# Performance work log

Measured on AMD Instinct MI355X. Metric: run time of the kernel, lower is better.

## Reference

```python
import jax, jax.numpy as jnp
import numpy as np

T, B, F, H, O = 512, 64, 128, 512, 16


def setup_inputs() -> dict:
    key = jax.random.key(0)
    ks = jax.random.split(key, 8)
    s = 1.0 / np.sqrt(H)  # torch RNN/Linear default uniform init scale
    u = lambda k, shape: jax.random.uniform(k, shape, jnp.float32, -s, s)
    return {
        "x_rnn": jax.random.normal(ks[0], (T, B, F), jnp.float32),
        "w_ih": u(ks[1], (3 * H, F)),   # gate order: r, z, n (PyTorch GRU)
        "w_hh": u(ks[2], (3 * H, H)),
        "b_ih": u(ks[3], (3 * H,)),
        "b_hh": u(ks[4], (3 * H,)),
        "w_out": u(ks[5], (O, H)),
        "b_out": u(ks[6], (O,)),
    }


def reference(x_rnn, w_ih, w_hh, b_ih, b_hh, w_out, b_out):
    # Single-layer GRU, seq-first (T, B, F), h0 = zeros (torch default when hx=None).
    h_dim = w_hh.shape[1]
    # Precompute all input-side gate pre-activations in one big GEMM: (T, B, 3H)
    xg = jnp.einsum("tbf,gf->tbg", x_rnn, w_ih) + b_ih

    def step(h, xg_t):
        hg = h @ w_hh.T + b_hh               # (B, 3H)
        xr, xz, xn = jnp.split(xg_t, 3, axis=-1)
        hr, hz, hn = jnp.split(hg, 3, axis=-1)
        r = jax.nn.sigmoid(xr + hr)
        z = jax.nn.sigmoid(xz + hz)
        n = jnp.tanh(xn + r * hn)
        h_new = (1.0 - z) * n + z * h
        return h_new, h_new

    h0 = jnp.zeros((x_rnn.shape[1], h_dim), x_rnn.dtype)
    _, hs = jax.lax.scan(step, h0, xg)       # hs: (T, B, H)
    # Output projection y = hs @ W_out^T + b_out -> (T, B, O)
    return jnp.einsum("tbh,oh->tbo", hs, w_out) + b_out
```

## Files before the change

kernel.cpp:

```cpp
#include <hip/hip_runtime.h>
#include <stdint.h>
#include <stddef.h>


#define T_LEN 512
#define B_SZ  64
#define F_DIM 128
#define H_DIM 512
#define O_DIM 16
#define SENTINEL 0xAAAAAAAAu

typedef __attribute__((ext_vector_type(8))) short short8;
typedef __attribute__((ext_vector_type(4))) float floatx4;
typedef __attribute__((ext_vector_type(4))) unsigned int uintx4;

__device__ __forceinline__ unsigned short f2bf(float f) {
  unsigned u = __builtin_bit_cast(unsigned, f);
  u += 0x7fffu + ((u >> 16) & 1u);
  return (unsigned short)(u >> 16);
}

__device__ __forceinline__ float fastrcp(float d) {
  float r = __builtin_amdgcn_rcpf(d);
  return r * (2.0f - d * r);
}

__device__ __forceinline__ float sigmoidf_(float x) {
  return fastrcp(1.0f + __expf(-x));
}

__device__ __forceinline__ float tanhf_(float x) {
  float v = fminf(fmaxf(x, -10.f), 10.f);
  float e = __expf(2.f * v);
  return (e - 1.f) * fastrcp(e + 1.f);
}

__device__ __forceinline__ short8 cvt8(floatx4 f0, floatx4 f1) {
  short8 a;
  a[0] = (short)f2bf(f0[0]); a[1] = (short)f2bf(f0[1]);
  a[2] = (short)f2bf(f0[2]); a[3] = (short)f2bf(f0[3]);
  a[4] = (short)f2bf(f1[0]); a[5] = (short)f2bf(f1[1]);
  a[6] = (short)f2bf(f1[2]); a[7] = (short)f2bf(f1[3]);
  return a;
}

__device__ __forceinline__ void hload4_sc1(floatx4* hf, const unsigned short* hbase) {
  asm volatile(
      "global_load_dwordx4 %0, %4, off sc1\n\t"
      "global_load_dwordx4 %1, %4, off offset:64 sc1\n\t"
      "global_load_dwordx4 %2, %4, off offset:128 sc1\n\t"
      "global_load_dwordx4 %3, %4, off offset:192 sc1\n\t"
      "s_waitcnt vmcnt(0)"
      : "=&v"(hf[0]), "=&v"(hf[1]), "=&v"(hf[2]), "=&v"(hf[3])
      : "v"(hbase)
      : "memory");
}

__global__ __launch_bounds__(256, 1)
void gru_persistent(const float* __restrict__ x,
                    const float* __restrict__ w_ih,
                    const float* __restrict__ w_hh,
                    const float* __restrict__ b_ih,
                    const float* __restrict__ b_hh,
                    unsigned short* __restrict__ hs) {
  __shared__ __align__(16) float part[2][4][16][33][4];

  const int tid  = threadIdx.x;
  const int lane = tid & 63;
  const int wv   = tid >> 6;
  const int bg   = blockIdx.x >> 4;
  const int cg   = blockIdx.x & 15;
  const int bgbase  = bg * 16;
  const int colbase = cg * 32;
  const int n16  = lane & 15;
  const int quad = lane >> 4;

  short8 bwx[3][2];
  short8 bwh[3][2][4];
  #pragma unroll
  for (int g = 0; g < 3; ++g) {
    #pragma unroll
    for (int nt = 0; nt < 2; ++nt) {
      const int grow = g * H_DIM + colbase + nt * 16 + n16;
      const float* pih = w_ih + (size_t)grow * F_DIM + wv * 32 + quad * 8;
      {
        short8 v;
        #pragma unroll
        for (int j = 0; j < 8; ++j) v[j] = (short)f2bf(pih[j]);
        bwx[g][nt] = v;
      }
      const float* phh = w_hh + (size_t)grow * H_DIM + wv * 128 + quad * 8;
      #pragma unroll
      for (int i = 0; i < 4; ++i) {
        short8 v;
        #pragma unroll
        for (int j = 0; j < 8; ++j) v[j] = (short)f2bf(phh[i * 32 + j]);
        bwh[g][nt][i] = v;
      }
    }
  }

  const int ew_b  = tid >> 4;
  const int ew_j0 = (tid & 15) * 2;
  float b_rz[2], b_zz[2], b_in[2], b_hn[2];
  #pragma unroll
  for (int e = 0; e < 2; ++e) {
    const int c = colbase + ew_j0 + e;
    b_rz[e] = b_ih[c] + b_hh[c];
    b_zz[e] = b_ih[H_DIM + c] + b_hh[H_DIM + c];
    b_in[e] = b_ih[2 * H_DIM + c];
    b_hn[e] = b_hh[2 * H_DIM + c];
  }
  float hm[2] = {0.0f, 0.0f};

  floatx4 xf0, xf1;
  {
    const float* px = x + ((size_t)(bgbase + n16)) * F_DIM + wv * 32 + quad * 8;
    xf0 = *(const floatx4*)px;
    xf1 = *(const floatx4*)(px + 4);
  }

  int mguard = 1 << 18;

  for (int t = 0; t < T_LEN; ++t) {
    floatx4 aR0 = {0.f,0.f,0.f,0.f}, aR1 = {0.f,0.f,0.f,0.f};
    floatx4 aZ0 = {0.f,0.f,0.f,0.f}, aZ1 = {0.f,0.f,0.f,0.f};
    floatx4 aX0 = {0.f,0.f,0.f,0.f}, aX1 = {0.f,0.f,0.f,0.f};
    floatx4 aH0 = {0.f,0.f,0.f,0.f}, aH1 = {0.f,0.f,0.f,0.f};
    {
      short8 a = cvt8(xf0, xf1);
      aR0 = __builtin_amdgcn_mfma_f32_16x16x32_bf16(a, bwx[0][0], aR0, 0, 0, 0);
      aR1 = __builtin_amdgcn_mfma_f32_16x16x32_bf16(a, bwx[0][1], aR1, 0, 0, 0);
      aZ0 = __builtin_amdgcn_mfma_f32_16x16x32_bf16(a, bwx[1][0], aZ0, 0, 0, 0);
      aZ1 = __builtin_amdgcn_mfma_f32_16x16x32_bf16(a, bwx[1][1], aZ1, 0, 0, 0);
      aX0 = __builtin_amdgcn_mfma_f32_16x16x32_bf16(a, bwx[2][0], aX0, 0, 0, 0);
      aX1 = __builtin_amdgcn_mfma_f32_16x16x32_bf16(a, bwx[2][1], aX1, 0, 0, 0);
    }

    if (t > 0) {
      floatx4 hf[4];
      {
        const unsigned short* hbase =
            hs + ((size_t)((t - 1) * B_SZ + bgbase + n16)) * H_DIM + wv * 128 + quad * 8;
        while (true) {
          hload4_sc1(hf, hbase);
          bool ok = true;
          #pragma unroll
          for (int i = 0; i < 4; ++i) {
            uintx4 u = __builtin_bit_cast(uintx4, hf[i]);
            ok = ok && (u[0] != SENTINEL) && (u[1] != SENTINEL) &&
                       (u[2] != SENTINEL) && (u[3] != SENTINEL);
          }
          if (__ballot(!ok) == 0ull) break;
          if (--mguard <= 0) break;
        }
      }
      if (t + 1 < T_LEN) {
        const float* px = x + ((size_t)((t + 1) * B_SZ + bgbase + n16)) * F_DIM +
                          wv * 32 + quad * 8;
        xf0 = *(const floatx4*)px;
        xf1 = *(const floatx4*)(px + 4);
      }
      #pragma unroll
      for (int i = 0; i < 4; ++i) {
        short8 a = __builtin_bit_cast(short8, hf[i]);
        aR0 = __builtin_amdgcn_mfma_f32_16x16x32_bf16(a, bwh[0][0][i], aR0, 0, 0, 0);
        aR1 = __builtin_amdgcn_mfma_f32_16x16x32_bf16(a, bwh[0][1][i], aR1, 0, 0, 0);
        aZ0 = __builtin_amdgcn_mfma_f32_16x16x32_bf16(a, bwh[1][0][i], aZ0, 0, 0, 0);
        aZ1 = __builtin_amdgcn_mfma_f32_16x16x32_bf16(a, bwh[1][1][i], aZ1, 0, 0, 0);
        aH0 = __builtin_amdgcn_mfma_f32_16x16x32_bf16(a, bwh[2][0][i], aH0, 0, 0, 0);
        aH1 = __builtin_amdgcn_mfma_f32_16x16x32_bf16(a, bwh[2][1][i], aH1, 0, 0, 0);
      }
    } else {
      const float* px = x + ((size_t)(B_SZ + bgbase + n16)) * F_DIM + wv * 32 + quad * 8;
      xf0 = *(const floatx4*)px;
      xf1 = *(const floatx4*)(px + 4);
    }

    {
      const int tb = t & 1;
      #pragma unroll
      for (int i = 0; i < 4; ++i) {
        const int r = quad * 4 + i;
        floatx4 v0 = {aR0[i], aZ0[i], aX0[i], aH0[i]};
        floatx4 v1 = {aR1[i], aZ1[i], aX1[i], aH1[i]};
        *(floatx4*)&part[tb][wv][r][n16][0]      = v0;
        *(floatx4*)&part[tb][wv][r][16 + n16][0] = v1;
      }
    }
    __syncthreads();

    {
      const int tb = t & 1;
      float pr[2] = {0.f, 0.f}, pz[2] = {0.f, 0.f};
      float pn[2] = {0.f, 0.f}, ph[2] = {0.f, 0.f};
      #pragma unroll
      for (int w = 0; w < 4; ++w) {
        #pragma unroll
        for (int e = 0; e < 2; ++e) {
          floatx4 g = *(const floatx4*)&part[tb][w][ew_b][ew_j0 + e][0];
          pr[e] += g[0]; pz[e] += g[1]; pn[e] += g[2]; ph[e] += g[3];
        }
      }
      unsigned short hb[2];
      #pragma unroll
      for (int e = 0; e < 2; ++e) {
        const float r = sigmoidf_(pr[e] + b_rz[e]);
        const float z = sigmoidf_(pz[e] + b_zz[e]);
        const float n = tanhf_(pn[e] + b_in[e] + r * (ph[e] + b_hn[e]));
        const float hn2 = (1.0f - z) * n + z * hm[e];
        hm[e] = hn2;
        hb[e] = f2bf(hn2);
      }
      const unsigned int packed = ((unsigned int)hb[1] << 16) | (unsigned int)hb[0];
      unsigned int* dst = (unsigned int*)(hs +
          ((size_t)(t * B_SZ + bgbase + ew_b)) * H_DIM + colbase + ew_j0);
      __hip_atomic_store(dst, packed, __ATOMIC_RELAXED, __HIP_MEMORY_SCOPE_AGENT);
    }
  }
}

__global__ __launch_bounds__(256, 1)
void gru_proj(const unsigned short* __restrict__ hs,
              const float* __restrict__ w_out,
              const float* __restrict__ b_out,
              float* __restrict__ y) {
  const int tid  = threadIdx.x;
  const int lane = tid & 63;
  const int wv   = tid >> 6;
  const int n16  = lane & 15;
  const int quad = lane >> 4;
  const size_t rowbase = ((size_t)blockIdx.x * 4 + wv) * 16;

  short8 bw[16];
  const float* pw = w_out + (size_t)n16 * H_DIM + quad * 8;
  #pragma unroll
  for (int kc = 0; kc < 16; ++kc) {
    short8 v;
    #pragma unroll
    for (int j = 0; j < 8; ++j) v[j] = (short)f2bf(pw[kc * 32 + j]);
    bw[kc] = v;
  }
  const float bo = b_out[n16];

  const unsigned short* hbase = hs + (rowbase + n16) * H_DIM + quad * 8;
  floatx4 acc = {0.f, 0.f, 0.f, 0.f};
  #pragma unroll
  for (int kc = 0; kc < 16; ++kc) {
    short8 a = *(const short8*)(hbase + kc * 32);
    acc = __builtin_amdgcn_mfma_f32_16x16x32_bf16(a, bw[kc], acc, 0, 0, 0);
  }
  #pragma unroll
  for (int i = 0; i < 4; ++i) {
    const size_t r = rowbase + quad * 4 + i;
    y[r * O_DIM + n16] = acc[i] + bo;
  }
}

extern "C" void kernel_launch(void* const* d_in, const int* in_sizes, int n_in,
                              void* d_out, int out_size, void* d_ws, size_t ws_size,
                              hipStream_t stream) {
  (void)in_sizes; (void)n_in; (void)out_size; (void)ws_size;
  const float* x     = (const float*)d_in[0];
  const float* w_ih  = (const float*)d_in[1];
  const float* w_hh  = (const float*)d_in[2];
  const float* b_ih  = (const float*)d_in[3];
  const float* b_hh  = (const float*)d_in[4];
  const float* w_out = (const float*)d_in[5];
  const float* b_out = (const float*)d_in[6];
  float* y = (float*)d_out;

  unsigned short* hs = (unsigned short*)d_ws;

  gru_persistent<<<64, 256, 0, stream>>>(x, w_ih, w_hh, b_ih, b_hh, hs);
  gru_proj<<<(T_LEN * B_SZ) / 16 / 4, 256, 0, stream>>>(hs, w_out, b_out, y);
}
```

Measured before the change: 1.080 ms.

## Interleave two batch groups per persistent block to hide cross-block sync latency

Halves the persistent grid so each block owns two 16-row batch groups. Each timestep now runs group A's step and then group B's step in alternation. While one group polls for the other blocks' hidden-state slices from the previous step, those producers have had a whole group-step of time to publish them. The aim is to hide the inter-block polling latency, at the cost of doubling the serial per-block work per timestep and using fewer CUs.

Result: slower. 1.831 ms (+69.6%).

```diff
diff --git a/kernel.cpp b/kernel.cpp
--- a/kernel.cpp
+++ b/kernel.cpp
@@ -13,6 +13,8 @@
 typedef __attribute__((ext_vector_type(8))) short short8;
 typedef __attribute__((ext_vector_type(4))) float floatx4;
 typedef __attribute__((ext_vector_type(4))) unsigned int uintx4;
+
+#define MFMA16(a, b, c) __builtin_amdgcn_mfma_f32_16x16x32_bf16((a), (b), (c), 0, 0, 0)
 
 __device__ __forceinline__ unsigned short f2bf(float f) {
   unsigned u = __builtin_bit_cast(unsigned, f);
@@ -56,24 +58,37 @@
       : "memory");
 }
 
+__device__ __forceinline__ bool clean4(const floatx4* hf) {
+  bool ok = true;
+  #pragma unroll
+  for (int i = 0; i < 4; ++i) {
+    uintx4 u = __builtin_bit_cast(uintx4, hf[i]);
+    ok = ok & (u[0] != SENTINEL) & (u[1] != SENTINEL) &
+         (u[2] != SENTINEL) & (u[3] != SENTINEL);
+  }
+  return __ballot(!ok) == 0ull;
+}
+
 __global__ __launch_bounds__(256, 1)
-void gru_persistent(const float* __restrict__ x,
-                    const float* __restrict__ w_ih,
-                    const float* __restrict__ w_hh,
-                    const float* __restrict__ b_ih,
-                    const float* __restrict__ b_hh,
-                    unsigned short* __restrict__ hs) {
+void gru_persistent2(const float* __restrict__ x,
+                     const float* __restrict__ w_ih,
+                     const float* __restrict__ w_hh,
+                     const float* __restrict__ b_ih,
+                     const float* __restrict__ b_hh,
+                     unsigned short* __restrict__ hs) {
   __shared__ __align__(16) float part[2][4][16][33][4];
 
   const int tid  = threadIdx.x;
   const int lane = tid & 63;
   const int wv   = tid >> 6;
-  const int bg   = blockIdx.x >> 4;
   const int cg   = blockIdx.x & 15;
-  const int bgbase  = bg * 16;
+  const int pair = blockIdx.x >> 4;
+  const int bgA  = pair * 32;
+  const int bgB  = bgA + 16;
   const int colbase = cg * 32;
   const int n16  = lane & 15;
   const int quad = lane >> 4;
+  const floatx4 fz = {0.f, 0.f, 0.f, 0.f};
 
   short8 bwx[3][2];
   short8 bwh[3][2][4];
@@ -111,111 +126,119 @@
     b_in[e] = b_ih[2 * H_DIM + c];
     b_hn[e] = b_hh[2 * H_DIM + c];
   }
-  float hm[2] = {0.0f, 0.0f};
-
-  floatx4 xf0, xf1;
+  float hmA[2] = {0.f, 0.f}, hmB[2] = {0.f, 0.f};
+
+  floatx4 xfA0, xfA1, xfB0, xfB1;
   {
-    const float* px = x + ((size_t)(bgbase + n16)) * F_DIM + wv * 32 + quad * 8;
-    xf0 = *(const floatx4*)px;
-    xf1 = *(const floatx4*)(px + 4);
-  }
-
+    const float* pa = x + ((size_t)(bgA + n16)) * F_DIM + wv * 32 + quad * 8;
+    xfA0 = *(const floatx4*)pa; xfA1 = *(const floatx4*)(pa + 4);
+    const float* pb = x + ((size_t)(bgB + n16)) * F_DIM + wv * 32 + quad * 8;
+    xfB0 = *(const floatx4*)pb; xfB1 = *(const floatx4*)(pb + 4);
+  }
+
+  floatx4 acc[8];
+  floatx4 hf[4];
   int mguard = 1 << 18;
 
-  for (int t = 0; t < T_LEN; ++t) {
-    floatx4 aR0 = {0.f,0.f,0.f,0.f}, aR1 = {0.f,0.f,0.f,0.f};
-    floatx4 aZ0 = {0.f,0.f,0.f,0.f}, aZ1 = {0.f,0.f,0.f,0.f};
-    floatx4 aX0 = {0.f,0.f,0.f,0.f}, aX1 = {0.f,0.f,0.f,0.f};
-    floatx4 aH0 = {0.f,0.f,0.f,0.f}, aH1 = {0.f,0.f,0.f,0.f};
-    {
-      short8 a = cvt8(xf0, xf1);
-      aR0 = __builtin_amdgcn_mfma_f32_16x16x32_bf16(a, bwx[0][0], aR0, 0, 0, 0);
-      aR1 = __builtin_amdgcn_mfma_f32_16x16x32_bf16(a, bwx[0][1], aR1, 0, 0, 0);
-      aZ0 = __builtin_amdgcn_mfma_f32_16x16x32_bf16(a, bwx[1][0], aZ0, 0, 0, 0);
-      aZ1 = __builtin_amdgcn_mfma_f32_16x16x32_bf16(a, bwx[1][1], aZ1, 0, 0, 0);
-      aX0 = __builtin_amdgcn_mfma_f32_16x16x32_bf16(a, bwx[2][0], aX0, 0, 0, 0);
-      aX1 = __builtin_amdgcn_mfma_f32_16x16x32_bf16(a, bwx[2][1], aX1, 0, 0, 0);
-    }
-
-    if (t > 0) {
-      floatx4 hf[4];
-      {
-        const unsigned short* hbase =
-            hs + ((size_t)((t - 1) * B_SZ + bgbase + n16)) * H_DIM + wv * 128 + quad * 8;
-        while (true) {
-          hload4_sc1(hf, hbase);
-          bool ok = true;
-          #pragma unroll
-          for (int i = 0; i < 4; ++i) {
-            uintx4 u = __builtin_bit_cast(uintx4, hf[i]);
-            ok = ok && (u[0] != SENTINEL) && (u[1] != SENTINEL) &&
-                       (u[2] != SENTINEL) && (u[3] != SENTINEL);
-          }
-          if (__ballot(!ok) == 0ull) break;
-          if (--mguard <= 0) break;
-        }
-      }
-      if (t + 1 < T_LEN) {
-        const float* px = x + ((size_t)((t + 1) * B_SZ + bgbase + n16)) * F_DIM +
-                          wv * 32 + quad * 8;
-        xf0 = *(const floatx4*)px;
-        xf1 = *(const floatx4*)(px + 4);
-      }
-      #pragma unroll
-      for (int i = 0; i < 4; ++i) {
-        short8 a = __builtin_bit_cast(short8, hf[i]);
-        aR0 = __builtin_amdgcn_mfma_f32_16x16x32_bf16(a, bwh[0][0][i], aR0, 0, 0, 0);
-        aR1 = __builtin_amdgcn_mfma_f32_16x16x32_bf16(a, bwh[0][1][i], aR1, 0, 0, 0);
-        aZ0 = __builtin_amdgcn_mfma_f32_16x16x32_bf16(a, bwh[1][0][i], aZ0, 0, 0, 0);
-        aZ1 = __builtin_amdgcn_mfma_f32_16x16x32_bf16(a, bwh[1][1][i], aZ1, 0, 0, 0);
-        aH0 = __builtin_amdgcn_mfma_f32_16x16x32_bf16(a, bwh[2][0][i], aH0, 0, 0, 0);
-        aH1 = __builtin_amdgcn_mfma_f32_16x16x32_bf16(a, bwh[2][1][i], aH1, 0, 0, 0);
-      }
-    } else {
-      const float* px = x + ((size_t)(B_SZ + bgbase + n16)) * F_DIM + wv * 32 + quad * 8;
-      xf0 = *(const floatx4*)px;
-      xf1 = *(const floatx4*)(px + 4);
-    }
-
-    {
-      const int tb = t & 1;
-      #pragma unroll
-      for (int i = 0; i < 4; ++i) {
-        const int r = quad * 4 + i;
-        floatx4 v0 = {aR0[i], aZ0[i], aX0[i], aH0[i]};
-        floatx4 v1 = {aR1[i], aZ1[i], aX1[i], aH1[i]};
-        *(floatx4*)&part[tb][wv][r][n16][0]      = v0;
-        *(floatx4*)&part[tb][wv][r][16 + n16][0] = v1;
-      }
+  auto xpart = [&](short8 a) {
+    acc[0] = MFMA16(a, bwx[0][0], fz); acc[1] = MFMA16(a, bwx[0][1], fz);
+    acc[2] = MFMA16(a, bwx[1][0], fz); acc[3] = MFMA16(a, bwx[1][1], fz);
+    acc[4] = MFMA16(a, bwx[2][0], fz); acc[5] = MFMA16(a, bwx[2][1], fz);
+    acc[6] = fz; acc[7] = fz;
+  };
+  auto hpart = [&]() {
+    #pragma unroll
+    for (int i = 0; i < 4; ++i) {
+      short8 a = __builtin_bit_cast(short8, hf[i]);
+      acc[0] = MFMA16(a, bwh[0][0][i], acc[0]); acc[1] = MFMA16(a, bwh[0][1][i], acc[1]);
+      acc[2] = MFMA16(a, bwh[1][0][i], acc[2]); acc[3] = MFMA16(a, bwh[1][1][i], acc[3]);
+      acc[6] = MFMA16(a, bwh[2][0][i], acc[6]); acc[7] = MFMA16(a, bwh[2][1][i], acc[7]);
+    }
+  };
+  auto epilogue = [&](int pb, int bgbase, float* hm2, int t) {
+    #pragma unroll
+    for (int i = 0; i < 4; ++i) {
+      const int r = quad * 4 + i;
+      floatx4 v0 = {acc[0][i], acc[2][i], acc[4][i], acc[6][i]};
+      floatx4 v1 = {acc[1][i], acc[3][i], acc[5][i], acc[7][i]};
+      *(floatx4*)&part[pb][wv][r][n16][0]      = v0;
+      *(floatx4*)&part[pb][wv][r][16 + n16][0] = v1;
     }
     __syncthreads();
-
-    {
-      const int tb = t & 1;
-      float pr[2] = {0.f, 0.f}, pz[2] = {0.f, 0.f};
-      float pn[2] = {0.f, 0.f}, ph[2] = {0.f, 0.f};
-      #pragma unroll
-      for (int w = 0; w < 4; ++w) {
-        #pragma unroll
-        for (int e = 0; e < 2; ++e) {
-          floatx4 g = *(const floatx4*)&part[tb][w][ew_b][ew_j0 + e][0];
-          pr[e] += g[0]; pz[e] += g[1]; pn[e] += g[2]; ph[e] += g[3];
-        }
-      }
-      unsigned short hb[2];
+    float pr[2] = {0.f, 0.f}, pz[2] = {0.f, 0.f};
+    float pn[2] = {0.f, 0.f}, ph[2] = {0.f, 0.f};
+    #pragma unroll
+    for (int w = 0; w < 4; ++w) {
       #pragma unroll
       for (int e = 0; e < 2; ++e) {
-        const float r = sigmoidf_(pr[e] + b_rz[e]);
-        const float z = sigmoidf_(pz[e] + b_zz[e]);
-        const float n = tanhf_(pn[e] + b_in[e] + r * (ph[e] + b_hn[e]));
-        const float hn2 = (1.0f - z) * n + z * hm[e];
-        hm[e] = hn2;
-        hb[e] = f2bf(hn2);
-      }
-      const unsigned int packed = ((unsigned int)hb[1] << 16) | (unsigned int)hb[0];
-      unsigned int* dst = (unsigned int*)(hs +
-          ((size_t)(t * B_SZ + bgbase + ew_b)) * H_DIM + colbase + ew_j0);
-      __hip_atomic_store(dst, packed, __ATOMIC_RELAXED, __HIP_MEMORY_SCOPE_AGENT);
+        floatx4 g = *(const floatx4*)&part[pb][w][ew_b][ew_j0 + e][0];
+        pr[e] += g[0]; pz[e] += g[1]; pn[e] += g[2]; ph[e] += g[3];
+      }
+    }
+    unsigned short hb2[2];
+    #pragma unroll
+    for (int e = 0; e < 2; ++e) {
+      const float r = sigmoidf_(pr[e] + b_rz[e]);
+      const float z = sigmoidf_(pz[e] + b_zz[e]);
+      const float n = tanhf_(pn[e] + b_in[e] + r * (ph[e] + b_hn[e]));
+      const float hn2 = (1.0f - z) * n + z * hm2[e];
+      hm2[e] = hn2;
+      hb2[e] = f2bf(hn2);
+    }
+    const unsigned int packed = ((unsigned int)hb2[1] << 16) | (unsigned int)hb2[0];
+    unsigned int* dst = (unsigned int*)(hs +
+        ((size_t)(t * B_SZ + bgbase + ew_b)) * H_DIM + colbase + ew_j0);
+    __hip_atomic_store(dst, packed, __ATOMIC_RELAXED, __HIP_MEMORY_SCOPE_AGENT);
+  };
+
+  xpart(cvt8(xfA0, xfA1));
+  {
+    const float* p = x + ((size_t)(B_SZ + bgA + n16)) * F_DIM + wv * 32 + quad * 8;
+    xfA0 = *(const floatx4*)p; xfA1 = *(const floatx4*)(p + 4);
+  }
+  epilogue(0, bgA, hmA, 0);
+
+  xpart(cvt8(xfB0, xfB1));
+  {
+    const float* p = x + ((size_t)(B_SZ + bgB + n16)) * F_DIM + wv * 32 + quad * 8;
+    xfB0 = *(const floatx4*)p; xfB1 = *(const floatx4*)(p + 4);
+  }
+  epilogue(1, bgB, hmB, 0);
+
+  for (int t = 1; t < T_LEN; ++t) {
+    {
+      xpart(cvt8(xfA0, xfA1));
+      const unsigned short* hb =
+          hs + ((size_t)((t - 1) * B_SZ + bgA + n16)) * H_DIM + wv * 128 + quad * 8;
+      while (true) {
+        hload4_sc1(hf, hb);
+        if (clean4(hf)) break;
+        if (--mguard <= 0) break;
+      }
+      if (t + 1 < T_LEN) {
+        const float* p = x + ((size_t)((t + 1) * B_SZ + bgA + n16)) * F_DIM +
+                         wv * 32 + quad * 8;
+        xfA0 = *(const floatx4*)p; xfA1 = *(const floatx4*)(p + 4);
+      }
+      hpart();
+      epilogue(0, bgA, hmA, t);
+    }
+    {
+      xpart(cvt8(xfB0, xfB1));
+      const unsigned short* hb =
+          hs + ((size_t)((t - 1) * B_SZ + bgB + n16)) * H_DIM + wv * 128 + quad * 8;
+      while (true) {
+        hload4_sc1(hf, hb);
+        if (clean4(hf)) break;
+        if (--mguard <= 0) break;
+      }
+      if (t + 1 < T_LEN) {
+        const float* p = x + ((size_t)((t + 1) * B_SZ + bgB + n16)) * F_DIM +
+                         wv * 32 + quad * 8;
+        xfB0 = *(const floatx4*)p; xfB1 = *(const floatx4*)(p + 4);
+      }
+      hpart();
+      epilogue(1, bgB, hmB, t);
     }
   }
 }
@@ -248,7 +271,7 @@
   #pragma unroll
   for (int kc = 0; kc < 16; ++kc) {
     short8 a = *(const short8*)(hbase + kc * 32);
-    acc = __builtin_amdgcn_mfma_f32_16x16x32_bf16(a, bw[kc], acc, 0, 0, 0);
+    acc = MFMA16(a, bw[kc], acc);
   }
   #pragma unroll
   for (int i = 0; i < 4; ++i) {
@@ -272,6 +295,6 @@
 
   unsigned short* hs = (unsigned short*)d_ws;
 
-  gru_persistent<<<64, 256, 0, stream>>>(x, w_ih, w_hh, b_ih, b_hh, hs);
+  gru_persistent2<<<32, 256, 0, stream>>>(x, w_ih, w_hh, b_ih, b_hh, hs);
   gru_proj<<<(T_LEN * B_SZ) / 16 / 4, 256, 0, stream>>>(hs, w_out, b_out, y);
 }
```

## Remap blocks to XCD slots and try cheaper sc0 polling before sc1

Applied to the files above, without the earlier changes.

Launches 128 blocks but keeps only those whose index mod 8 is below 4. Each batch group's column blocks then land on the same XCD under round-robin dispatch, which is meant to keep h exchange within one L2. The poll loop first tries up to three sc0 loads and clean checks before falling back to sc1 loads. It turns sc0 off after step 6 if it rarely succeeds. Each h store is also issued a second time with a plain global_store_dword, which adds memory traffic and relies on the hardware block-to-XCD mapping assumption.

Result: slower. 1.643 ms (+52.2%).

```diff
diff --git a/kernel.cpp b/kernel.cpp
--- a/kernel.cpp
+++ b/kernel.cpp
@@ -13,6 +13,8 @@
 typedef __attribute__((ext_vector_type(8))) short short8;
 typedef __attribute__((ext_vector_type(4))) float floatx4;
 typedef __attribute__((ext_vector_type(4))) unsigned int uintx4;
+
+#define MFMA16(a, b, c) __builtin_amdgcn_mfma_f32_16x16x32_bf16((a), (b), (c), 0, 0, 0)
 
 __device__ __forceinline__ unsigned short f2bf(float f) {
   unsigned u = __builtin_bit_cast(unsigned, f);
@@ -56,6 +58,29 @@
       : "memory");
 }
 
+__device__ __forceinline__ void hload4_sc0(floatx4* hf, const unsigned short* hbase) {
+  asm volatile(
+      "global_load_dwordx4 %0, %4, off sc0\n\t"
+      "global_load_dwordx4 %1, %4, off offset:64 sc0\n\t"
+      "global_load_dwordx4 %2, %4, off offset:128 sc0\n\t"
+      "global_load_dwordx4 %3, %4, off offset:192 sc0\n\t"
+      "s_waitcnt vmcnt(0)"
+      : "=&v"(hf[0]), "=&v"(hf[1]), "=&v"(hf[2]), "=&v"(hf[3])
+      : "v"(hbase)
+      : "memory");
+}
+
+__device__ __forceinline__ bool clean4(const floatx4* hf) {
+  bool ok = true;
+  #pragma unroll
+  for (int i = 0; i < 4; ++i) {
+    uintx4 u = __builtin_bit_cast(uintx4, hf[i]);
+    ok = ok & (u[0] != SENTINEL) & (u[1] != SENTINEL) &
+         (u[2] != SENTINEL) & (u[3] != SENTINEL);
+  }
+  return __ballot(!ok) == 0ull;
+}
+
 __global__ __launch_bounds__(256, 1)
 void gru_persistent(const float* __restrict__ x,
                     const float* __restrict__ w_ih,
@@ -63,13 +88,16 @@
                     const float* __restrict__ b_ih,
                     const float* __restrict__ b_hh,
                     unsigned short* __restrict__ hs) {
+  const int slot = (int)blockIdx.x & 7;
+  if (slot >= 4) return;
+
   __shared__ __align__(16) float part[2][4][16][33][4];
 
   const int tid  = threadIdx.x;
   const int lane = tid & 63;
   const int wv   = tid >> 6;
-  const int bg   = blockIdx.x >> 4;
-  const int cg   = blockIdx.x & 15;
+  const int bg   = slot;
+  const int cg   = (int)blockIdx.x >> 3;
   const int bgbase  = bg * 16;
   const int colbase = cg * 32;
   const int n16  = lane & 15;
@@ -120,7 +148,9 @@
     xf1 = *(const floatx4*)(px + 4);
   }
 
-  int mguard = 1 << 18;
+  int mguard  = 1 << 18;
+  int use_sc0 = 1;
+  int s0wins  = 0;
 
   for (int t = 0; t < T_LEN; ++t) {
     floatx4 aR0 = {0.f,0.f,0.f,0.f}, aR1 = {0.f,0.f,0.f,0.f};
@@ -129,12 +159,9 @@
     floatx4 aH0 = {0.f,0.f,0.f,0.f}, aH1 = {0.f,0.f,0.f,0.f};
     {
       short8 a = cvt8(xf0, xf1);
-      aR0 = __builtin_amdgcn_mfma_f32_16x16x32_bf16(a, bwx[0][0], aR0, 0, 0, 0);
-      aR1 = __builtin_amdgcn_mfma_f32_16x16x32_bf16(a, bwx[0][1], aR1, 0, 0, 0);
-      aZ0 = __builtin_amdgcn_mfma_f32_16x16x32_bf16(a, bwx[1][0], aZ0, 0, 0, 0);
-      aZ1 = __builtin_amdgcn_mfma_f32_16x16x32_bf16(a, bwx[1][1], aZ1, 0, 0, 0);
-      aX0 = __builtin_amdgcn_mfma_f32_16x16x32_bf16(a, bwx[2][0], aX0, 0, 0, 0);
-      aX1 = __builtin_amdgcn_mfma_f32_16x16x32_bf16(a, bwx[2][1], aX1, 0, 0, 0);
+      aR0 = MFMA16(a, bwx[0][0], aR0); aR1 = MFMA16(a, bwx[0][1], aR1);
+      aZ0 = MFMA16(a, bwx[1][0], aZ0); aZ1 = MFMA16(a, bwx[1][1], aZ1);
+      aX0 = MFMA16(a, bwx[2][0], aX0); aX1 = MFMA16(a, bwx[2][1], aX1);
     }
 
     if (t > 0) {
@@ -142,17 +169,22 @@
       {
         const unsigned short* hbase =
             hs + ((size_t)((t - 1) * B_SZ + bgbase + n16)) * H_DIM + wv * 128 + quad * 8;
+        bool won0 = false;
+        int tries = use_sc0 ? 3 : 0;
         while (true) {
-          hload4_sc1(hf, hbase);
-          bool ok = true;
-          #pragma unroll
-          for (int i = 0; i < 4; ++i) {
-            uintx4 u = __builtin_bit_cast(uintx4, hf[i]);
-            ok = ok && (u[0] != SENTINEL) && (u[1] != SENTINEL) &&
-                       (u[2] != SENTINEL) && (u[3] != SENTINEL);
+          if (tries > 0) {
+            --tries;
+            hload4_sc0(hf, hbase);
+            if (clean4(hf)) { won0 = true; break; }
+          } else {
+            hload4_sc1(hf, hbase);
+            if (clean4(hf)) break;
           }
-          if (__ballot(!ok) == 0ull) break;
           if (--mguard <= 0) break;
+        }
+        if (t <= 6) {
+          s0wins += (int)won0;
+          if (t == 6 && s0wins < 3) use_sc0 = 0;
         }
       }
       if (t + 1 < T_LEN) {
@@ -164,12 +196,9 @@
       #pragma unroll
       for (int i = 0; i < 4; ++i) {
         short8 a = __builtin_bit_cast(short8, hf[i]);
-        aR0 = __builtin_amdgcn_mfma_f32_16x16x32_bf16(a, bwh[0][0][i], aR0, 0, 0, 0);
-        aR1 = __builtin_amdgcn_mfma_f32_16x16x32_bf16(a, bwh[0][1][i], aR1, 0, 0, 0);
-        aZ0 = __builtin_amdgcn_mfma_f32_16x16x32_bf16(a, bwh[1][0][i], aZ0, 0, 0, 0);
-        aZ1 = __builtin_amdgcn_mfma_f32_16x16x32_bf16(a, bwh[1][1][i], aZ1, 0, 0, 0);
-        aH0 = __builtin_amdgcn_mfma_f32_16x16x32_bf16(a, bwh[2][0][i], aH0, 0, 0, 0);
-        aH1 = __builtin_amdgcn_mfma_f32_16x16x32_bf16(a, bwh[2][1][i], aH1, 0, 0, 0);
+        aR0 = MFMA16(a, bwh[0][0][i], aR0); aR1 = MFMA16(a, bwh[0][1][i], aR1);
+        aZ0 = MFMA16(a, bwh[1][0][i], aZ0); aZ1 = MFMA16(a, bwh[1][1][i], aZ1);
+        aH0 = MFMA16(a, bwh[2][0][i], aH0); aH1 = MFMA16(a, bwh[2][1][i], aH1);
       }
     } else {
       const float* px = x + ((size_t)(B_SZ + bgbase + n16)) * F_DIM + wv * 32 + quad * 8;
@@ -216,6 +245,8 @@
       unsigned int* dst = (unsigned int*)(hs +
           ((size_t)(t * B_SZ + bgbase + ew_b)) * H_DIM + colbase + ew_j0);
       __hip_atomic_store(dst, packed, __ATOMIC_RELAXED, __HIP_MEMORY_SCOPE_AGENT);
+      asm volatile("global_store_dword %0, %1, off"
+                   :: "v"(dst), "v"(packed) : "memory");
     }
   }
 }
@@ -248,7 +279,7 @@
   #pragma unroll
   for (int kc = 0; kc < 16; ++kc) {
     short8 a = *(const short8*)(hbase + kc * 32);
-    acc = __builtin_amdgcn_mfma_f32_16x16x32_bf16(a, bw[kc], acc, 0, 0, 0);
+    acc = MFMA16(a, bw[kc], acc);
   }
   #pragma unroll
   for (int i = 0; i < 4; ++i) {
@@ -272,6 +303,6 @@
 
   unsigned short* hs = (unsigned short*)d_ws;
 
-  gru_persistent<<<64, 256, 0, stream>>>(x, w_ih, w_hh, b_ih, b_hh, hs);
+  gru_persistent<<<128, 256, 0, stream>>>(x, w_ih, w_hh, b_ih, b_hh, hs);
   gru_proj<<<(T_LEN * B_SZ) / 16 / 4, 256, 0, stream>>>(hs, w_out, b_out, y);
 }
```

## Give each wave full-K GRU tiles to drop LDS reduction and block barrier

Applied to the files above, without the earlier changes.

Restructures the persistent GRU so each wavefront owns a 16-batch by 16-column tile across the full hidden and input K dimensions, instead of splitting K across four waves and reducing partials through shared memory with __syncthreads. The gate math runs directly on MFMA accumulators, and bf16 pairs are packed via lane shuffle before the atomic store. The grid goes from 64 blocks to 32 blocks of 4 independent waves, so 128 waves each spin-poll for the previous step's h. The cost is that each wave now holds all 16 K-chunks of w_hh per gate in registers, roughly 192 VGPRs for weights, which raises register pressure and risks spills. Each wave also runs a longer serial MFMA chain per step.

Result: slower. 3.682 ms (+240.9%).

```diff
diff --git a/kernel.cpp b/kernel.cpp
--- a/kernel.cpp
+++ b/kernel.cpp
@@ -13,6 +13,8 @@
 typedef __attribute__((ext_vector_type(8))) short short8;
 typedef __attribute__((ext_vector_type(4))) float floatx4;
 typedef __attribute__((ext_vector_type(4))) unsigned int uintx4;
+
+#define MFMA16(a, b, c) __builtin_amdgcn_mfma_f32_16x16x32_bf16((a), (b), (c), 0, 0, 0)
 
 __device__ __forceinline__ unsigned short f2bf(float f) {
   unsigned u = __builtin_bit_cast(unsigned, f);
@@ -44,178 +46,145 @@
   return a;
 }
 
-__device__ __forceinline__ void hload4_sc1(floatx4* hf, const unsigned short* hbase) {
+__device__ __forceinline__ void hissue4(floatx4* hf, const unsigned short* hbase) {
   asm volatile(
       "global_load_dwordx4 %0, %4, off sc1\n\t"
       "global_load_dwordx4 %1, %4, off offset:64 sc1\n\t"
       "global_load_dwordx4 %2, %4, off offset:128 sc1\n\t"
-      "global_load_dwordx4 %3, %4, off offset:192 sc1\n\t"
-      "s_waitcnt vmcnt(0)"
+      "global_load_dwordx4 %3, %4, off offset:192 sc1"
       : "=&v"(hf[0]), "=&v"(hf[1]), "=&v"(hf[2]), "=&v"(hf[3])
       : "v"(hbase)
       : "memory");
 }
 
 __global__ __launch_bounds__(256, 1)
-void gru_persistent(const float* __restrict__ x,
-                    const float* __restrict__ w_ih,
-                    const float* __restrict__ w_hh,
-                    const float* __restrict__ b_ih,
-                    const float* __restrict__ b_hh,
-                    unsigned short* __restrict__ hs) {
-  __shared__ __align__(16) float part[2][4][16][33][4];
-
+void gru_wave(const float* __restrict__ x,
+              const float* __restrict__ w_ih,
+              const float* __restrict__ w_hh,
+              const float* __restrict__ b_ih,
+              const float* __restrict__ b_hh,
+              unsigned short* __restrict__ hs) {
   const int tid  = threadIdx.x;
   const int lane = tid & 63;
   const int wv   = tid >> 6;
-  const int bg   = blockIdx.x >> 4;
-  const int cg   = blockIdx.x & 15;
+  const int unit = (int)blockIdx.x * 4 + wv;
+  const int bg   = unit & 3;
+  const int ct   = unit >> 2;
   const int bgbase  = bg * 16;
-  const int colbase = cg * 32;
+  const int colbase = ct * 16;
   const int n16  = lane & 15;
   const int quad = lane >> 4;
-
-  short8 bwx[3][2];
-  short8 bwh[3][2][4];
+  const floatx4 fz = {0.f, 0.f, 0.f, 0.f};
+
+  short8 bwh[3][16];
+  short8 bwx[3][4];
   #pragma unroll
   for (int g = 0; g < 3; ++g) {
-    #pragma unroll
-    for (int nt = 0; nt < 2; ++nt) {
-      const int grow = g * H_DIM + colbase + nt * 16 + n16;
-      const float* pih = w_ih + (size_t)grow * F_DIM + wv * 32 + quad * 8;
-      {
-        short8 v;
+    const int grow = g * H_DIM + colbase + n16;
+    const float* phh = w_hh + (size_t)grow * H_DIM + quad * 8;
+    #pragma unroll
+    for (int kc = 0; kc < 16; ++kc) {
+      short8 v;
+      #pragma unroll
+      for (int j = 0; j < 8; ++j) v[j] = (short)f2bf(phh[kc * 32 + j]);
+      bwh[g][kc] = v;
+    }
+    const float* pih = w_ih + (size_t)grow * F_DIM + quad * 8;
+    #pragma unroll
+    for (int kc = 0; kc < 4; ++kc) {
+      short8 v;
+      #pragma unroll
+      for (int j = 0; j < 8; ++j) v[j] = (short)f2bf(pih[kc * 32 + j]);
+      bwx[g][kc] = v;
+    }
+  }
+
+  const int c = colbase + n16;
+  const float b_rz = b_ih[c] + b_hh[c];
+  const float b_zz = b_ih[H_DIM + c] + b_hh[H_DIM + c];
+  const float b_in = b_ih[2 * H_DIM + c];
+  const float b_hn = b_hh[2 * H_DIM + c];
+  float hm[4] = {0.f, 0.f, 0.f, 0.f};
+
+  short8 ax[4];
+  {
+    const float* px = x + ((size_t)(bgbase + n16)) * F_DIM + quad * 8;
+    #pragma unroll
+    for (int kc = 0; kc < 4; ++kc)
+      ax[kc] = cvt8(*(const floatx4*)(px + kc * 32),
+                    *(const floatx4*)(px + kc * 32 + 4));
+  }
+
+  floatx4 hv[16];
+  int mguard = 1 << 18;
+
+  for (int t = 0; t < T_LEN; ++t) {
+    floatx4 aR = fz, aZ = fz, aX = fz, aH = fz;
+    #pragma unroll
+    for (int kc = 0; kc < 4; ++kc) {
+      aR = MFMA16(ax[kc], bwx[0][kc], aR);
+      aZ = MFMA16(ax[kc], bwx[1][kc], aZ);
+      aX = MFMA16(ax[kc], bwx[2][kc], aX);
+    }
+
+    if (t > 0) {
+      const unsigned short* hb =
+          hs + ((size_t)((t - 1) * B_SZ + bgbase + n16)) * H_DIM + quad * 8;
+      while (true) {
+        hissue4(hv + 0,  hb);
+        hissue4(hv + 4,  hb + 128);
+        hissue4(hv + 8,  hb + 256);
+        hissue4(hv + 12, hb + 384);
+        asm volatile("s_waitcnt vmcnt(0)" ::: "memory");
+        __builtin_amdgcn_sched_barrier(0);
+        bool ok = true;
         #pragma unroll
-        for (int j = 0; j < 8; ++j) v[j] = (short)f2bf(pih[j]);
-        bwx[g][nt] = v;
-      }
-      const float* phh = w_hh + (size_t)grow * H_DIM + wv * 128 + quad * 8;
-      #pragma unroll
-      for (int i = 0; i < 4; ++i) {
-        short8 v;
-        #pragma unroll
-        for (int j = 0; j < 8; ++j) v[j] = (short)f2bf(phh[i * 32 + j]);
-        bwh[g][nt][i] = v;
-      }
-    }
-  }
-
-  const int ew_b  = tid >> 4;
-  const int ew_j0 = (tid & 15) * 2;
-  float b_rz[2], b_zz[2], b_in[2], b_hn[2];
-  #pragma unroll
-  for (int e = 0; e < 2; ++e) {
-    const int c = colbase + ew_j0 + e;
-    b_rz[e] = b_ih[c] + b_hh[c];
-    b_zz[e] = b_ih[H_DIM + c] + b_hh[H_DIM + c];
-    b_in[e] = b_ih[2 * H_DIM + c];
-    b_hn[e] = b_hh[2 * H_DIM + c];
-  }
-  float hm[2] = {0.0f, 0.0f};
-
-  floatx4 xf0, xf1;
-  {
-    const float* px = x + ((size_t)(bgbase + n16)) * F_DIM + wv * 32 + quad * 8;
-    xf0 = *(const floatx4*)px;
-    xf1 = *(const floatx4*)(px + 4);
-  }
-
-  int mguard = 1 << 18;
-
-  for (int t = 0; t < T_LEN; ++t) {
-    floatx4 aR0 = {0.f,0.f,0.f,0.f}, aR1 = {0.f,0.f,0.f,0.f};
-    floatx4 aZ0 = {0.f,0.f,0.f,0.f}, aZ1 = {0.f,0.f,0.f,0.f};
-    floatx4 aX0 = {0.f,0.f,0.f,0.f}, aX1 = {0.f,0.f,0.f,0.f};
-    floatx4 aH0 = {0.f,0.f,0.f,0.f}, aH1 = {0.f,0.f,0.f,0.f};
-    {
-      short8 a = cvt8(xf0, xf1);
-      aR0 = __builtin_amdgcn_mfma_f32_16x16x32_bf16(a, bwx[0][0], aR0, 0, 0, 0);
-      aR1 = __builtin_amdgcn_mfma_f32_16x16x32_bf16(a, bwx[0][1], aR1, 0, 0, 0);
-      aZ0 = __builtin_amdgcn_mfma_f32_16x16x32_bf16(a, bwx[1][0], aZ0, 0, 0, 0);
-      aZ1 = __builtin_amdgcn_mfma_f32_16x16x32_bf16(a, bwx[1][1], aZ1, 0, 0, 0);
-      aX0 = __builtin_amdgcn_mfma_f32_16x16x32_bf16(a, bwx[2][0], aX0, 0, 0, 0);
-      aX1 = __builtin_amdgcn_mfma_f32_16x16x32_bf16(a, bwx[2][1], aX1, 0, 0, 0);
-    }
-
-    if (t > 0) {
-      floatx4 hf[4];
-      {
-        const unsigned short* hbase =
-            hs + ((size_t)((t - 1) * B_SZ + bgbase + n16)) * H_DIM + wv * 128 + quad * 8;
-        while (true) {
-          hload4_sc1(hf, hbase);
-          bool ok = true;
-          #pragma unroll
-          for (int i = 0; i < 4; ++i) {
-            uintx4 u = __builtin_bit_cast(uintx4, hf[i]);
-            ok = ok && (u[0] != SENTINEL) && (u[1] != SENTINEL) &&
-                       (u[2] != SENTINEL) && (u[3] != SENTINEL);
-          }
-          if (__ballot(!ok) == 0ull) break;
-          if (--mguard <= 0) break;
+        for (int i = 0; i < 16; ++i) {
+          uintx4 u = __builtin_bit_cast(uintx4, hv[i]);
+          ok = ok && (u[0] != SENTINEL) && (u[1] != SENTINEL) &&
+                     (u[2] != SENTINEL) && (u[3] != SENTINEL);
         }
+        if (__ballot(!ok) == 0ull) break;
+        if (--mguard <= 0) break;
       }
       if (t + 1 < T_LEN) {
         const float* px = x + ((size_t)((t + 1) * B_SZ + bgbase + n16)) * F_DIM +
-                          wv * 32 + quad * 8;
-        xf0 = *(const floatx4*)px;
-        xf1 = *(const floatx4*)(px + 4);
-      }
-      #pragma unroll
-      for (int i = 0; i < 4; ++i) {
-        short8 a = __builtin_bit_cast(short8, hf[i]);
-        aR0 = __builtin_amdgcn_mfma_f32_16x16x32_bf16(a, bwh[0][0][i], aR0, 0, 0, 0);
-        aR1 = __builtin_amdgcn_mfma_f32_16x16x32_bf16(a, bwh[0][1][i], aR1, 0, 0, 0);
-        aZ0 = __builtin_amdgcn_mfma_f32_16x16x32_bf16(a, bwh[1][0][i], aZ0, 0, 0, 0);
-        aZ1 = __builtin_amdgcn_mfma_f32_16x16x32_bf16(a, bwh[1][1][i], aZ1, 0, 0, 0);
-        aH0 = __builtin_amdgcn_mfma_f32_16x16x32_bf16(a, bwh[2][0][i], aH0, 0, 0, 0);
-        aH1 = __builtin_amdgcn_mfma_f32_16x16x32_bf16(a, bwh[2][1][i], aH1, 0, 0, 0);
-      }
-    } else {
-      const float* px = x + ((size_t)(B_SZ + bgbase + n16)) * F_DIM + wv * 32 + quad * 8;
-      xf0 = *(const floatx4*)px;
-      xf1 = *(const floatx4*)(px + 4);
-    }
-
-    {
-      const int tb = t & 1;
-      #pragma unroll
-      for (int i = 0; i < 4; ++i) {
-        const int r = quad * 4 + i;
-        floatx4 v0 = {aR0[i], aZ0[i], aX0[i], aH0[i]};
-        floatx4 v1 = {aR1[i], aZ1[i], aX1[i], aH1[i]};
-        *(floatx4*)&part[tb][wv][r][n16][0]      = v0;
-        *(floatx4*)&part[tb][wv][r][16 + n16][0] = v1;
-      }
-    }
-    __syncthreads();
-
-    {
-      const int tb = t & 1;
-      float pr[2] = {0.f, 0.f}, pz[2] = {0.f, 0.f};
-      float pn[2] = {0.f, 0.f}, ph[2] = {0.f, 0.f};
-      #pragma unroll
-      for (int w = 0; w < 4; ++w) {
+                          quad * 8;
         #pragma unroll
-        for (int e = 0; e < 2; ++e) {
-          floatx4 g = *(const floatx4*)&part[tb][w][ew_b][ew_j0 + e][0];
-          pr[e] += g[0]; pz[e] += g[1]; pn[e] += g[2]; ph[e] += g[3];
-        }
-      }
-      unsigned short hb[2];
-      #pragma unroll
-      for (int e = 0; e < 2; ++e) {
-        const float r = sigmoidf_(pr[e] + b_rz[e]);
-        const float z = sigmoidf_(pz[e] + b_zz[e]);
-        const float n = tanhf_(pn[e] + b_in[e] + r * (ph[e] + b_hn[e]));
-        const float hn2 = (1.0f - z) * n + z * hm[e];
-        hm[e] = hn2;
-        hb[e] = f2bf(hn2);
-      }
-      const unsigned int packed = ((unsigned int)hb[1] << 16) | (unsigned int)hb[0];
-      unsigned int* dst = (unsigned int*)(hs +
-          ((size_t)(t * B_SZ + bgbase + ew_b)) * H_DIM + colbase + ew_j0);
-      __hip_atomic_store(dst, packed, __ATOMIC_RELAXED, __HIP_MEMORY_SCOPE_AGENT);
+        for (int kc = 0; kc < 4; ++kc)
+          ax[kc] = cvt8(*(const floatx4*)(px + kc * 32),
+                        *(const floatx4*)(px + kc * 32 + 4));
+      }
+      #pragma unroll
+      for (int kc = 0; kc < 16; ++kc) {
+        short8 a = __builtin_bit_cast(short8, hv[kc]);
+        aR = MFMA16(a, bwh[0][kc], aR);
+        aZ = MFMA16(a, bwh[1][kc], aZ);
+        aH = MFMA16(a, bwh[2][kc], aH);
+      }
+    } else if (T_LEN > 1) {
+      const float* px = x + ((size_t)(B_SZ + bgbase + n16)) * F_DIM + quad * 8;
+      #pragma unroll
+      for (int kc = 0; kc < 4; ++kc)
+        ax[kc] = cvt8(*(const floatx4*)(px + kc * 32),
+                      *(const floatx4*)(px + kc * 32 + 4));
+    }
+
+    #pragma unroll
+    for (int i = 0; i < 4; ++i) {
+      const float r = sigmoidf_(aR[i] + b_rz);
+      const float z = sigmoidf_(aZ[i] + b_zz);
+      const float n = tanhf_(aX[i] + b_in + r * (aH[i] + b_hn));
+      const float hn2 = (1.0f - z) * n + z * hm[i];
+      hm[i] = hn2;
+      const unsigned int mine  = (unsigned int)f2bf(hn2);
+      const unsigned int other = (unsigned int)__shfl_xor((int)mine, 1);
+      if ((n16 & 1) == 0) {
+        const unsigned int packed = (other << 16) | mine;
+        unsigned int* dst = (unsigned int*)(hs +
+            ((size_t)(t * B_SZ + bgbase + quad * 4 + i)) * H_DIM + colbase + n16);
+        __hip_atomic_store(dst, packed, __ATOMIC_RELAXED, __HIP_MEMORY_SCOPE_AGENT);
+      }
     }
   }
 }
@@ -248,7 +217,7 @@
   #pragma unroll
   for (int kc = 0; kc < 16; ++kc) {
     short8 a = *(const short8*)(hbase + kc * 32);
-    acc = __builtin_amdgcn_mfma_f32_16x16x32_bf16(a, bw[kc], acc, 0, 0, 0);
+    acc = MFMA16(a, bw[kc], acc);
   }
   #pragma unroll
   for (int i = 0; i < 4; ++i) {
@@ -272,6 +241,6 @@
 
   unsigned short* hs = (unsigned short*)d_ws;
 
-  gru_persistent<<<64, 256, 0, stream>>>(x, w_ih, w_hh, b_ih, b_hh, hs);
+  gru_wave<<<32, 256, 0, stream>>>(x, w_ih, w_hh, b_ih, b_hh, hs);
   gru_proj<<<(T_LEN * B_SZ) / 16 / 4, 256, 0, stream>>>(hs, w_out, b_out, y);
 }
```
